# Optimization experiments

Measured on AMD Instinct MI355X. Metric: run time of the kernel, lower is better.

The kernel has to match this reference:

```python
import jax, jax.numpy as jnp
import numpy as np

BINS = 256
EPS = 1e-8


def _norm255(x):
    # (x - min) / (max - min) * 255, truncated to int (torch .int())
    mx = jnp.max(x, axis=(2, 3), keepdims=True)
    mn = jnp.min(x, axis=(2, 3), keepdims=True)
    return ((x - mn) / (mx - mn) * 255.0).astype(jnp.int32)


def _hist256(x):
    # x int32 [B,C,H,W] -> per-(b,c) 256-bin histogram [B,C,256] float32
    B, C = x.shape[0], x.shape[1]
    flat = x.reshape(B * C, -1)
    rows = jnp.arange(B * C)[:, None]
    h = jnp.zeros((B * C, BINS), jnp.float32).at[rows, flat].add(1.0)
    return h.reshape(B, C, BINS)


def _entropy(x):
    # faithful to Entropy(): p = hist / (H*W); h = -sum p*log(p+1e-8)
    B, C, H, W = x.shape
    p = _hist256(x) / (H * W)
    h = -jnp.sum(p * jnp.log(p + EPS), axis=2)
    return h[:, :, None, None]  # [B,C,1,1]


def _joint_entropy(x_p, x_ms):
    # Faithful to Joint_entropy's quirky count: for each (i,j) it counts pixels
    # where (x_ms==i AND x_p==j) OR (x_ms!=i AND x_p!=j).
    # count[i,j] = 2*J[i,j] + npix - hist_ms[i] - hist_p[j], J = joint histogram.
    B, C, H, W = x_ms.shape
    npix = H * W
    bins = jnp.arange(BINS)
    M = (x_ms.reshape(B, C, npix)[..., None] == bins).astype(jnp.float32)  # [B,C,P,256]
    P = (x_p.reshape(B, npix)[..., None] == bins).astype(jnp.float32)      # [B,P,256]
    J = jnp.einsum('bcpi,bpj->bcij', M, P)                                  # [B,C,256,256]
    hist_ms = jnp.sum(M, axis=2)  # [B,C,256]
    hist_p = jnp.sum(P, axis=1)   # [B,256]
    count = 2.0 * J + npix - hist_ms[:, :, :, None] - hist_p[:, None, None, :]
    p = count / float(BINS * BINS)  # original divides by 256*256, not npix
    h = -jnp.sum(p * jnp.log(p + EPS), axis=(2, 3))
    return h[:, :, None, None]  # [B,C,1,1]


def _channel(f_p, f_ms):
    B, C, H, W = f_p.shape
    f_p_m = jnp.mean(f_p, axis=1, keepdims=True)  # [B,1,H,W]
    # AdaptiveAvgPool2d((16,16)) with H,W divisible by 16 == block mean
    pooled = f_p.reshape(B, C, 16, H // 16, 16, W // 16).mean(axis=(3, 5))
    f_p_a = jnp.mean(pooled, axis=1, keepdims=True)  # [B,1,16,16]
    f_ms_n = _norm255(f_ms)
    f_p_m_n = _norm255(f_p_m)
    f_p_a_n = _norm255(f_p_a)
    h_ms = _entropy(f_ms_n)                 # [B,C,1,1]
    h_p = _entropy(f_p_m_n)                 # [B,1,1,1]
    h_ms_p = _joint_entropy(f_p_a_n, f_ms_n)  # [B,C,1,1]
    mi = h_p + h_ms - h_ms_p
    mi = jax.nn.softmax(mi, axis=1)  # nn.Softmax() on 4D -> dim=1
    return f_ms + f_ms * mi


def _similarity(f_p, f_ms):
    B, C, H, W = f_p.shape
    f_ms_u = jax.image.resize(f_ms, (B, C, H, W), method='bilinear')
    a = f_ms_u.reshape(B, C, -1)
    b = f_p.reshape(B, C, -1)
    a = a - jnp.mean(a, axis=2, keepdims=True)
    b = b - jnp.mean(b, axis=2, keepdims=True)
    na = jnp.sqrt(jnp.sum(a * a, axis=2))  # [B,C] (ms norms)
    nb = jnp.sqrt(jnp.sum(b * b, axis=2))  # [B,C] (p norms)
    s = jnp.einsum('bcp,bdp->bcd', a, b)   # [B,C,C]
    return s / ((na * nb) / 100.0)[:, :, None]


def _spatial(f_p, f_ms):
    B, C, H, W = f_p.shape
    s_m = _similarity(f_p, f_ms)
    mx = jnp.max(s_m, axis=2)        # [B,C]
    idx = jnp.argmax(s_m, axis=2)    # [B,C] best f_p channel per ms channel
    scores = jax.nn.softmax(mx, axis=1)
    brow = jnp.arange(B)[:, None]
    # group score: sum of softmax scores of ms-channels that picked value v
    g = jnp.zeros((B, C), scores.dtype).at[brow, idx].add(scores)
    cnt = jnp.zeros((B, C), jnp.int32).at[brow, idx].add(1)
    k = jnp.min(jnp.sum(cnt > 0, axis=1))  # min #unique over batch
    min_k = (k + 1) // 2                   # ceil(min_k / 2)
    order = jnp.argsort(-g, axis=1)        # descending group score; absent groups (0) sort last
    sorted_scores = jnp.take_along_axis(g, order, axis=1)  # [B,C]
    pos_mask = jnp.arange(C) < min_k       # keep top min_k positions
    z = jnp.where(pos_mask[None, :], sorted_scores, -jnp.inf)
    w = jax.nn.softmax(z, axis=1)          # softmax over selected scores, 0 elsewhere
    gathered = jnp.take_along_axis(f_p, order[:, :, None, None], axis=1)  # [B,C,H,W]
    mask = jnp.sum(w[:, :, None, None] * jax.nn.sigmoid(gathered), axis=1, keepdims=True)
    return f_p + f_p * mask


def setup_inputs() -> dict:
    key = jax.random.key(0)
    k1, k2 = jax.random.split(key)
    f_p = jax.random.normal(k1, (8, 64, 256, 256), dtype=jnp.float32)
    f_ms = jax.random.normal(k2, (8, 64, 16, 16), dtype=jnp.float32)
    return {"f_p": f_p, "f_ms": f_ms}


def reference(f_p, f_ms):
    rel_ms = _channel(f_p, f_ms)
    rel_p = _spatial(f_p, f_ms)
    return (rel_p, rel_ms)
```

## Files before the change

### kernel.cpp

```cpp
#include <hip/hip_runtime.h>

#define BB 8
#define CC 64
#define HP 256
#define WP 256
#define PP 65536
#define QQ 256

__device__ __forceinline__ unsigned encF(float f) {
    unsigned u = __float_as_uint(f);
    return (u & 0x80000000u) ? ~u : (u | 0x80000000u);
}
__device__ __forceinline__ float decF(unsigned u) {
    unsigned b = (u & 0x80000000u) ? (u ^ 0x80000000u) : ~u;
    return __uint_as_float(b);
}

__device__ __forceinline__ double blockSumD(double v, double* red4) {
    int t = threadIdx.x;
    for (int d = 32; d; d >>= 1) v += __shfl_down(v, d, 64);
    __syncthreads();
    if ((t & 63) == 0) red4[t >> 6] = v;
    __syncthreads();
    double r = red4[0] + red4[1] + red4[2] + red4[3];
    __syncthreads();
    return r;
}

__global__ void k0_init(unsigned* minmax, int* histpm) {
    int t = threadIdx.x + blockIdx.x * blockDim.x;
    if (t < BB) { minmax[2 * t] = 0xFFFFFFFFu; minmax[2 * t + 1] = 0u; }
    if (t < BB * 256) histpm[t] = 0;
}

__global__ __launch_bounds__(256) void k1_fpm(const float* __restrict__ fp,
                                              float* __restrict__ fpm,
                                              unsigned* __restrict__ minmax) {
    int b = blockIdx.y;
    int i4 = blockIdx.x * 256 + threadIdx.x;
    const float4* src = (const float4*)(fp + (size_t)b * CC * PP);
    float sx = 0.f, sy = 0.f, sz = 0.f, sw = 0.f;
#pragma unroll 8
    for (int c = 0; c < CC; ++c) {
        float4 v = src[(size_t)c * (PP / 4) + i4];
        sx += v.x; sy += v.y; sz += v.z; sw += v.w;
    }
    const float inv = 1.0f / 64.0f;
    float4 m; m.x = sx * inv; m.y = sy * inv; m.z = sz * inv; m.w = sw * inv;
    ((float4*)(fpm + (size_t)b * PP))[i4] = m;
    float mn = fminf(fminf(m.x, m.y), fminf(m.z, m.w));
    float mx = fmaxf(fmaxf(m.x, m.y), fmaxf(m.z, m.w));
    for (int d = 32; d; d >>= 1) {
        mn = fminf(mn, __shfl_down(mn, d, 64));
        mx = fmaxf(mx, __shfl_down(mx, d, 64));
    }
    __shared__ unsigned smn, smx;
    if (threadIdx.x == 0) { smn = 0xFFFFFFFFu; smx = 0u; }
    __syncthreads();
    if ((threadIdx.x & 63) == 0) { atomicMin(&smn, encF(mn)); atomicMax(&smx, encF(mx)); }
    __syncthreads();
    if (threadIdx.x == 0) { atomicMin(&minmax[2 * b], smn); atomicMax(&minmax[2 * b + 1], smx); }
}

__global__ __launch_bounds__(256) void k2a_hist(const float* __restrict__ fpm,
                                                const unsigned* __restrict__ minmax,
                                                int* __restrict__ histpm) {
    int b = blockIdx.y;
    __shared__ int h[256];
    h[threadIdx.x] = 0;
    __syncthreads();
    float mn = decF(minmax[2 * b]);
    float mx = decF(minmax[2 * b + 1]);
    float dd = mx - mn;
    int i4 = blockIdx.x * 256 + threadIdx.x;
    float4 v = ((const float4*)(fpm + (size_t)b * PP))[i4];
    int b0 = (int)((v.x - mn) / dd * 255.0f);
    int b1 = (int)((v.y - mn) / dd * 255.0f);
    int b2 = (int)((v.z - mn) / dd * 255.0f);
    int b3 = (int)((v.w - mn) / dd * 255.0f);
    b0 = min(max(b0, 0), 255); b1 = min(max(b1, 0), 255);
    b2 = min(max(b2, 0), 255); b3 = min(max(b3, 0), 255);
    atomicAdd(&h[b0], 1); atomicAdd(&h[b1], 1);
    atomicAdd(&h[b2], 1); atomicAdd(&h[b3], 1);
    __syncthreads();
    atomicAdd(&histpm[b * 256 + threadIdx.x], h[threadIdx.x]);
}

__global__ __launch_bounds__(256) void k2b_entropy(const int* __restrict__ histpm,
                                                   float* __restrict__ hpE) {
    __shared__ double red4[4];
    int b = blockIdx.x;
    int n = histpm[b * 256 + threadIdx.x];
    float p = (float)n * (1.0f / 65536.0f);
    double term = -(double)(p * __logf(p + 1e-8f));
    double h = blockSumD(term, red4);
    if (threadIdx.x == 0) hpE[b] = (float)h;
}

__global__ __launch_bounds__(256) void k3_chan(const float* __restrict__ fp,
                                               float* __restrict__ cellsum,
                                               float* __restrict__ gtent,
                                               float* __restrict__ chsum,
                                               float* __restrict__ chsumsq) {
    int blk = blockIdx.x, b = blk >> 6, c = blk & 63;
    int x = threadIdx.x, s = x >> 4, r = x & 15;
    const float* src = fp + (size_t)(b * CC + c) * PP;
    __shared__ float tentL[256];
    __shared__ double red4[4];
    tentL[x] = 0.0f;
    __syncthreads();
    float wm, w0, wp;
    if (x <= 7)        { wm = 0.f; w0 = 1.f; wp = 0.f; }
    else if (x >= 248) { wm = 0.f; w0 = 1.f; wp = 0.f; }
    else if (r < 8)    { float fx = ((float)r + 8.5f) * 0.0625f; wm = 1.f - fx; w0 = fx;       wp = 0.f; }
    else               { float fx = ((float)r - 7.5f) * 0.0625f; wm = 0.f;      w0 = 1.f - fx; wp = fx;  }
    double sum = 0.0, ssq = 0.0;
    for (int q = 0; q < 16; ++q) {
        float am = 0.f, a0 = 0.f, ap = 0.f, cs = 0.f;
#pragma unroll
        for (int ry = 0; ry < 16; ++ry) {
            float v = src[(q * 16 + ry) * 256 + x];
            sum += (double)v;
            ssq += (double)v * (double)v;
            cs  += v;
            if ((q == 0 && ry < 8) || (q == 15 && ry >= 8)) {
                a0 += v;
            } else if (ry < 8) {
                float fy = ((float)ry + 8.5f) * 0.0625f;
                am += (1.f - fy) * v; a0 += fy * v;
            } else {
                float fy = ((float)ry - 7.5f) * 0.0625f;
                a0 += (1.f - fy) * v; ap += fy * v;
            }
        }
        float vals[10];
        vals[0] = am * wm; vals[1] = am * w0; vals[2] = am * wp;
        vals[3] = a0 * wm; vals[4] = a0 * w0; vals[5] = a0 * wp;
        vals[6] = ap * wm; vals[7] = ap * w0; vals[8] = ap * wp;
        vals[9] = cs;
#pragma unroll
        for (int d = 8; d; d >>= 1) {
#pragma unroll
            for (int k2 = 0; k2 < 10; ++k2) vals[k2] += __shfl_down(vals[k2], d, 16);
        }
        if (r == 0) {
            if (q > 0) {
                if (s > 0)  atomicAdd(&tentL[(q - 1) * 16 + (s - 1)], vals[0]);
                atomicAdd(&tentL[(q - 1) * 16 + s], vals[1]);
                if (s < 15) atomicAdd(&tentL[(q - 1) * 16 + (s + 1)], vals[2]);
            }
            if (s > 0)  atomicAdd(&tentL[q * 16 + (s - 1)], vals[3]);
            atomicAdd(&tentL[q * 16 + s], vals[4]);
            if (s < 15) atomicAdd(&tentL[q * 16 + (s + 1)], vals[5]);
            if (q < 15) {
                if (s > 0)  atomicAdd(&tentL[(q + 1) * 16 + (s - 1)], vals[6]);
                atomicAdd(&tentL[(q + 1) * 16 + s], vals[7]);
                if (s < 15) atomicAdd(&tentL[(q + 1) * 16 + (s + 1)], vals[8]);
            }
            cellsum[(size_t)(b * CC + c) * QQ + q * 16 + s] = vals[9];
        }
    }
    __syncthreads();
    gtent[(size_t)(b * CC + c) * QQ + x] = tentL[x];
    double st = blockSumD(sum, red4);
    double sq = blockSumD(ssq, red4);
    if (x == 0) { chsum[b * CC + c] = (float)st; chsumsq[b * CC + c] = (float)sq; }
}

__global__ __launch_bounds__(256) void k4_ms(const float* __restrict__ fms,
                                             int* __restrict__ msn,
                                             int* __restrict__ histms,
                                             float* __restrict__ hmsE,
                                             float* __restrict__ naArr,
                                             float* __restrict__ mssum) {
    int blk = blockIdx.x, b = blk >> 6, c = blk & 63, t = threadIdx.x;
    __shared__ float m[256];
    __shared__ int hist[256];
    __shared__ double red4[4];
    __shared__ double U[256];
    __shared__ unsigned umn, umx;
    float v = fms[(size_t)(b * CC + c) * QQ + t];
    m[t] = v;
    hist[t] = 0;
    if (t == 0) { umn = 0xFFFFFFFFu; umx = 0u; }
    float mn = v, mx = v;
    for (int d = 32; d; d >>= 1) {
        mn = fminf(mn, __shfl_down(mn, d, 64));
        mx = fmaxf(mx, __shfl_down(mx, d, 64));
    }
    __syncthreads();
    if ((t & 63) == 0) { atomicMin(&umn, encF(mn)); atomicMax(&umx, encF(mx)); }
    __syncthreads();
    mn = decF(umn); mx = decF(umx);
    int bin = (int)((v - mn) / (mx - mn) * 255.0f);
    bin = min(max(bin, 0), 255);
    msn[(size_t)(b * CC + c) * QQ + t] = bin;
    atomicAdd(&hist[bin], 1);
    __syncthreads();
    histms[(size_t)(b * CC + c) * QQ + t] = hist[t];
    float pf = (float)hist[t] * (1.0f / 256.0f);
    double term = -(double)(pf * __logf(pf + 1e-8f));
    double h = blockSumD(term, red4);
    if (t == 0) hmsE[b * CC + c] = (float)h;
    int i = t >> 4, j = t & 15;
    double kdj = (j == 0 || j == 15) ? 13.328125 : 10.65625;
    double mv = (double)m[t];
    double uu = kdj * mv + 2.671875 * ((j > 0 ? (double)m[t - 1] : 0.0) +
                                       (j < 15 ? (double)m[t + 1] : 0.0));
    U[t] = uu;
    __syncthreads();
    double kdi = (i == 0 || i == 15) ? 13.328125 : 10.65625;
    double vv = kdi * U[t] + 2.671875 * ((i > 0 ? U[t - 16] : 0.0) +
                                         (i < 15 ? U[t + 16] : 0.0));
    double sq = blockSumD(mv * vv, red4);
    double msm = blockSumD(mv, red4);
    if (t == 0) {
        mssum[b * CC + c] = (float)msm;
        double meanu = msm * (1.0 / 256.0);
        double na2 = sq - 65536.0 * meanu * meanu;
        naArr[b * CC + c] = (float)sqrt(na2 > 0.0 ? na2 : 0.0);
    }
}

__global__ __launch_bounds__(256) void k5_pa(const float* __restrict__ cellsum,
                                             int* __restrict__ pan,
                                             int* __restrict__ histp) {
    int b = blockIdx.x, t = threadIdx.x;
    __shared__ int hist[256];
    __shared__ unsigned umn, umx;
    hist[t] = 0;
    if (t == 0) { umn = 0xFFFFFFFFu; umx = 0u; }
    double acc = 0.0;
    for (int c = 0; c < CC; ++c) acc += (double)cellsum[(size_t)(b * CC + c) * QQ + t];
    float pa = (float)(acc * (1.0 / 256.0) * (1.0 / 64.0));
    float mn = pa, mx = pa;
    for (int d = 32; d; d >>= 1) {
        mn = fminf(mn, __shfl_down(mn, d, 64));
        mx = fmaxf(mx, __shfl_down(mx, d, 64));
    }
    __syncthreads();
    if ((t & 63) == 0) { atomicMin(&umn, encF(mn)); atomicMax(&umx, encF(mx)); }
    __syncthreads();
    mn = decF(umn); mx = decF(umx);
    int bin = (int)((pa - mn) / (mx - mn) * 255.0f);
    bin = min(max(bin, 0), 255);
    pan[b * QQ + t] = bin;
    atomicAdd(&hist[bin], 1);
    __syncthreads();
    histp[b * 256 + t] = hist[t];
}

__global__ __launch_bounds__(256) void k6_joint(const int* __restrict__ msn,
                                                const int* __restrict__ pan,
                                                const int* __restrict__ histms,
                                                const int* __restrict__ histp,
                                                float* __restrict__ hjoint) {
    int blk = blockIdx.x, b = blk >> 6, c = blk & 63, t = threadIdx.x;
    __shared__ int key[256], hms[256], hp[256];
    __shared__ double red4[4];
    int iv = msn[(size_t)(b * CC + c) * QQ + t];
    int jv = pan[b * QQ + t];
    key[t] = (iv << 8) | jv;
    hms[t] = histms[(size_t)(b * CC + c) * QQ + t];
    hp[t] = histp[b * 256 + t];
    __syncthreads();
    unsigned long long w0_ = 0, w1_ = 0, w2_ = 0, w3_ = 0;
    for (int p = 0; p < 256; ++p) {
        int k2 = key[p];
        if ((k2 >> 8) == t) {
            int j = k2 & 255;
            unsigned long long bit = 1ull << (j & 63);
            int w = j >> 6;
            if (w == 0) w0_ |= bit; else if (w == 1) w1_ |= bit;
            else if (w == 2) w2_ |= bit; else w3_ |= bit;
        }
    }
    double acc = 0.0;
    int basei = 256 - hms[t];
    unsigned long long words[4] = { w0_, w1_, w2_, w3_ };
#pragma unroll
    for (int w = 0; w < 4; ++w) {
        unsigned long long word = words[w];
        for (int jj = 0; jj < 64; ++jj) {
            if (!((word >> jj) & 1ull)) {
                int cnt = basei - hp[w * 64 + jj];
                float pf = (float)cnt * (1.0f / 65536.0f);
                acc -= (double)(pf * __logf(pf + 1e-8f));
            }
        }
    }
    int myk = key[t], n = 0; bool first = true;
    for (int p = 0; p < 256; ++p) {
        int k2 = key[p];
        if (k2 == myk) { n++; if (p < t) first = false; }
    }
    if (first) {
        int cnt = 2 * n + 256 - hms[myk >> 8] - hp[myk & 255];
        float pf = (float)cnt * (1.0f / 65536.0f);
        acc -= (double)(pf * __logf(pf + 1e-8f));
    }
    double h = blockSumD(acc, red4);
    if (t == 0) hjoint[b * CC + c] = (float)h;
}

__global__ __launch_bounds__(256) void k7_relms(const float* __restrict__ fms,
                                                const float* __restrict__ hmsE,
                                                const float* __restrict__ hpE,
                                                const float* __restrict__ hjoint,
                                                float* __restrict__ out2) {
    int b = blockIdx.x, t = threadIdx.x;
    __shared__ double mi[64];
    if (t < 64) mi[t] = (double)hpE[b] + (double)hmsE[b * CC + t] - (double)hjoint[b * CC + t];
    __syncthreads();
    if (t == 0) {
        double mxv = mi[0];
        for (int c2 = 1; c2 < 64; ++c2) if (mi[c2] > mxv) mxv = mi[c2];
        double s = 0.0;
        for (int c2 = 0; c2 < 64; ++c2) { mi[c2] = exp(mi[c2] - mxv); s += mi[c2]; }
        for (int c2 = 0; c2 < 64; ++c2) mi[c2] /= s;
    }
    __syncthreads();
    const float* src = fms + (size_t)b * CC * QQ;
    float* dst = out2 + (size_t)b * CC * QQ;
    for (int e = t; e < CC * QQ; e += 256) {
        float v = src[e];
        float miv = (float)mi[e >> 8];
        dst[e] = v + v * miv;
    }
}

__global__ __launch_bounds__(256) void k8_smax(const float* __restrict__ fms,
                                               const float* __restrict__ gtent,
                                               const float* __restrict__ mssum,
                                               const float* __restrict__ chsum,
                                               const float* __restrict__ chsumsq,
                                               const float* __restrict__ naArr,
                                               float* __restrict__ mxArr,
                                               int* __restrict__ idxArr) {
    int blk = blockIdx.x, b = blk >> 6, c = blk & 63, t = threadIdx.x;
    __shared__ float msrow[256];
    __shared__ double part[256];
    __shared__ double sval[64];
    msrow[t] = fms[(size_t)(b * CC + c) * QQ + t];
    __syncthreads();
    int d = t >> 2, pr = t & 3;
    const float* g = gtent + (size_t)(b * CC + d) * QQ + pr * 64;
    const float* mr = msrow + pr * 64;
    double acc = 0.0;
    for (int q2 = 0; q2 < 64; ++q2) acc += (double)mr[q2] * (double)g[q2];
    part[t] = acc;
    __syncthreads();
    if (t < 64) {
        double meanu = (double)mssum[b * CC + c] * (1.0 / 256.0);
        double meanp = (double)chsum[b * CC + t] * (1.0 / 65536.0);
        sval[t] = part[t * 4] + part[t * 4 + 1] + part[t * 4 + 2] + part[t * 4 + 3]
                  - 65536.0 * meanu * meanp;
    }
    __syncthreads();
    if (t == 0) {
        double best = sval[0]; int bi2 = 0;
        for (int dd = 1; dd < 64; ++dd) { if (sval[dd] > best) { best = sval[dd]; bi2 = dd; } }
        double nac = (double)naArr[b * CC + c];
        double sc_ = (double)chsum[b * CC + c];
        double sq_ = (double)chsumsq[b * CC + c];
        double nb2 = sq_ - sc_ * sc_ * (1.0 / 65536.0);
        double nbc = sqrt(nb2 > 0.0 ? nb2 : 0.0);
        mxArr[b * CC + c] = (float)(best * 100.0 / (nac * nbc));
        idxArr[b * CC + c] = bi2;
    }
}

__global__ __launch_bounds__(512) void k9_small(const float* __restrict__ mxArr,
                                                const int* __restrict__ idxArr,
                                                float* __restrict__ wsel,
                                                int* __restrict__ chanA,
                                                int* __restrict__ minkA) {
    __shared__ double sc[8][64];
    __shared__ double gs[8][64];
    __shared__ int idxS[8][64];
    __shared__ int ordv[8][64];
    __shared__ int uarr[8];
    __shared__ int mkS;
    int t = threadIdx.x;
    int b = t >> 6, c = t & 63;
    double v = (double)mxArr[b * 64 + c];
    double mx = v;
    for (int d = 32; d; d >>= 1) mx = fmax(mx, __shfl_down(mx, d, 64));
    mx = __shfl(mx, 0, 64);
    double e = exp(v - mx);
    double s = e;
    for (int d = 32; d; d >>= 1) s += __shfl_down(s, d, 64);
    s = __shfl(s, 0, 64);
    sc[b][c] = e / s;
    idxS[b][c] = idxArr[b * 64 + c];
    __syncthreads();
    double g = 0.0; int cnt = 0;
    for (int c2 = 0; c2 < 64; ++c2) {
        if (idxS[b][c2] == c) { g += sc[b][c2]; cnt++; }
    }
    gs[b][c] = g;
    unsigned long long ball = __ballot(cnt > 0);
    if (c == 0) uarr[b] = __popcll(ball);
    __syncthreads();
    if (t == 0) {
        int k = uarr[0];
        for (int b2 = 1; b2 < 8; ++b2) k = min(k, uarr[b2]);
        mkS = (k + 1) >> 1;
        minkA[0] = mkS;
    }
    __syncthreads();
    int rk = 0;
    double myg = gs[b][c];
    for (int c3 = 0; c3 < 64; ++c3) {
        double a = gs[b][c3];
        if (a > myg || (a == myg && c3 < c)) rk++;
    }
    ordv[b][rk] = c;
    __syncthreads();
    int mk = mkS;
    double z0 = gs[b][ordv[b][0]];
    double ee = (c < mk) ? exp(gs[b][ordv[b][c]] - z0) : 0.0;
    double se = ee;
    for (int d = 32; d; d >>= 1) se += __shfl_down(se, d, 64);
    se = __shfl(se, 0, 64);
    if (c < mk) {
        wsel[b * 64 + c] = (float)(ee / se);
        chanA[b * 64 + c] = ordv[b][c];
    }
}

__global__ __launch_bounds__(256) void k10_relp(const float* __restrict__ fp,
                                                const float* __restrict__ wsel,
                                                const int* __restrict__ chanA,
                                                const int* __restrict__ minkA,
                                                float* __restrict__ outp) {
    int b = blockIdx.y;
    int i4 = blockIdx.x * 256 + threadIdx.x;
    int mk = minkA[0];
    const float4* src = (const float4*)(fp + (size_t)b * CC * PP);
    float mx0 = 0.f, mx1 = 0.f, mx2 = 0.f, mx3 = 0.f;
    for (int i = 0; i < mk; ++i) {
        int ch = chanA[b * 64 + i];
        float wv = wsel[b * 64 + i];
        float4 v = src[(size_t)ch * (PP / 4) + i4];
        mx0 += wv * (1.0f / (1.0f + __expf(-v.x)));
        mx1 += wv * (1.0f / (1.0f + __expf(-v.y)));
        mx2 += wv * (1.0f / (1.0f + __expf(-v.z)));
        mx3 += wv * (1.0f / (1.0f + __expf(-v.w)));
    }
    float4* dst = (float4*)(outp + (size_t)b * CC * PP);
    for (int c2 = 0; c2 < CC; ++c2) {
        float4 v = src[(size_t)c2 * (PP / 4) + i4];
        float4 o;
        o.x = v.x + v.x * mx0;
        o.y = v.y + v.y * mx1;
        o.z = v.z + v.z * mx2;
        o.w = v.w + v.w * mx3;
        dst[(size_t)c2 * (PP / 4) + i4] = o;
    }
}

extern "C" void kernel_launch(void* const* d_in, const int* in_sizes, int n_in,
                              void* d_out, int out_size, void* d_ws, size_t ws_size,
                              hipStream_t stream) {
    const float* fp = (const float*)d_in[0];
    const float* fms = (const float*)d_in[1];
    float* out = (float*)d_out;

    char* p = (char*)d_ws;
    auto alloc = [&](size_t bytes) { void* r = (void*)p; p += (bytes + 255) & ~(size_t)255; return r; };

    float* fpm      = (float*)alloc((size_t)BB * PP * 4);
    float* cellsum  = (float*)alloc((size_t)BB * CC * QQ * 4);
    float* gtent    = (float*)alloc((size_t)BB * CC * QQ * 4);
    float* chsum    = (float*)alloc((size_t)BB * CC * 4);
    float* chsumsq  = (float*)alloc((size_t)BB * CC * 4);
    unsigned* minmax= (unsigned*)alloc((size_t)BB * 2 * 4);
    int* histpm     = (int*)alloc((size_t)BB * 256 * 4);
    int* msn        = (int*)alloc((size_t)BB * CC * QQ * 4);
    int* histms     = (int*)alloc((size_t)BB * CC * 256 * 4);
    int* histp      = (int*)alloc((size_t)BB * 256 * 4);
    int* pan        = (int*)alloc((size_t)BB * QQ * 4);
    float* hmsE     = (float*)alloc((size_t)BB * CC * 4);
    float* hpE      = (float*)alloc((size_t)BB * 4);
    float* hjoint   = (float*)alloc((size_t)BB * CC * 4);
    float* naArr    = (float*)alloc((size_t)BB * CC * 4);
    float* mssum    = (float*)alloc((size_t)BB * CC * 4);
    float* mxArr    = (float*)alloc((size_t)BB * CC * 4);
    int* idxArr     = (int*)alloc((size_t)BB * CC * 4);
    float* wsel     = (float*)alloc((size_t)BB * CC * 4);
    int* chanA      = (int*)alloc((size_t)BB * CC * 4);
    int* minkA      = (int*)alloc(256);

    float* out_relp  = out;
    float* out_relms = out + (size_t)BB * CC * PP;

    k0_init<<<8, 256, 0, stream>>>(minmax, histpm);
    k1_fpm<<<dim3(64, 8), 256, 0, stream>>>(fp, fpm, minmax);
    k2a_hist<<<dim3(64, 8), 256, 0, stream>>>(fpm, minmax, histpm);
    k2b_entropy<<<8, 256, 0, stream>>>(histpm, hpE);
    k3_chan<<<512, 256, 0, stream>>>(fp, cellsum, gtent, chsum, chsumsq);
    k4_ms<<<512, 256, 0, stream>>>(fms, msn, histms, hmsE, naArr, mssum);
    k5_pa<<<8, 256, 0, stream>>>(cellsum, pan, histp);
    k6_joint<<<512, 256, 0, stream>>>(msn, pan, histms, histp, hjoint);
    k7_relms<<<8, 256, 0, stream>>>(fms, hmsE, hpE, hjoint, out_relms);
    k8_smax<<<512, 256, 0, stream>>>(fms, gtent, mssum, chsum, chsumsq, naArr, mxArr, idxArr);
    k9_small<<<1, 512, 0, stream>>>(mxArr, idxArr, wsel, chanA, minkA);
    k10_relp<<<dim3(64, 8), 256, 0, stream>>>(fp, wsel, chanA, minkA, out_relp);
}
```

Baseline: 416.7 us.

## Fuse channel-mean pass into relp output kernel and merge small histogram kernels

```diff
diff --git a/kernel.cpp b/kernel.cpp
--- a/kernel.cpp
+++ b/kernel.cpp
@@ -27,74 +27,9 @@
     return r;
 }
 
-__global__ void k0_init(unsigned* minmax, int* histpm) {
-    int t = threadIdx.x + blockIdx.x * blockDim.x;
+__global__ __launch_bounds__(256) void k0_init(unsigned* __restrict__ minmax) {
+    int t = threadIdx.x;
     if (t < BB) { minmax[2 * t] = 0xFFFFFFFFu; minmax[2 * t + 1] = 0u; }
-    if (t < BB * 256) histpm[t] = 0;
-}
-
-__global__ __launch_bounds__(256) void k1_fpm(const float* __restrict__ fp,
-                                              float* __restrict__ fpm,
-                                              unsigned* __restrict__ minmax) {
-    int b = blockIdx.y;
-    int i4 = blockIdx.x * 256 + threadIdx.x;
-    const float4* src = (const float4*)(fp + (size_t)b * CC * PP);
-    float sx = 0.f, sy = 0.f, sz = 0.f, sw = 0.f;
-#pragma unroll 8
-    for (int c = 0; c < CC; ++c) {
-        float4 v = src[(size_t)c * (PP / 4) + i4];
-        sx += v.x; sy += v.y; sz += v.z; sw += v.w;
-    }
-    const float inv = 1.0f / 64.0f;
-    float4 m; m.x = sx * inv; m.y = sy * inv; m.z = sz * inv; m.w = sw * inv;
-    ((float4*)(fpm + (size_t)b * PP))[i4] = m;
-    float mn = fminf(fminf(m.x, m.y), fminf(m.z, m.w));
-    float mx = fmaxf(fmaxf(m.x, m.y), fmaxf(m.z, m.w));
-    for (int d = 32; d; d >>= 1) {
-        mn = fminf(mn, __shfl_down(mn, d, 64));
-        mx = fmaxf(mx, __shfl_down(mx, d, 64));
-    }
-    __shared__ unsigned smn, smx;
-    if (threadIdx.x == 0) { smn = 0xFFFFFFFFu; smx = 0u; }
-    __syncthreads();
-    if ((threadIdx.x & 63) == 0) { atomicMin(&smn, encF(mn)); atomicMax(&smx, encF(mx)); }
-    __syncthreads();
-    if (threadIdx.x == 0) { atomicMin(&minmax[2 * b], smn); atomicMax(&minmax[2 * b + 1], smx); }
-}
-
-__global__ __launch_bounds__(256) void k2a_hist(const float* __restrict__ fpm,
-                                                const unsigned* __restrict__ minmax,
-                                                int* __restrict__ histpm) {
-    int b = blockIdx.y;
-    __shared__ int h[256];
-    h[threadIdx.x] = 0;
-    __syncthreads();
-    float mn = decF(minmax[2 * b]);
-    float mx = decF(minmax[2 * b + 1]);
-    float dd = mx - mn;
-    int i4 = blockIdx.x * 256 + threadIdx.x;
-    float4 v = ((const float4*)(fpm + (size_t)b * PP))[i4];
-    int b0 = (int)((v.x - mn) / dd * 255.0f);
-    int b1 = (int)((v.y - mn) / dd * 255.0f);
-    int b2 = (int)((v.z - mn) / dd * 255.0f);
-    int b3 = (int)((v.w - mn) / dd * 255.0f);
-    b0 = min(max(b0, 0), 255); b1 = min(max(b1, 0), 255);
-    b2 = min(max(b2, 0), 255); b3 = min(max(b3, 0), 255);
-    atomicAdd(&h[b0], 1); atomicAdd(&h[b1], 1);
-    atomicAdd(&h[b2], 1); atomicAdd(&h[b3], 1);
-    __syncthreads();
-    atomicAdd(&histpm[b * 256 + threadIdx.x], h[threadIdx.x]);
-}
-
-__global__ __launch_bounds__(256) void k2b_entropy(const int* __restrict__ histpm,
-                                                   float* __restrict__ hpE) {
-    __shared__ double red4[4];
-    int b = blockIdx.x;
-    int n = histpm[b * 256 + threadIdx.x];
-    float p = (float)n * (1.0f / 65536.0f);
-    double term = -(double)(p * __logf(p + 1e-8f));
-    double h = blockSumD(term, red4);
-    if (threadIdx.x == 0) hpE[b] = (float)h;
 }
 
 __global__ __launch_bounds__(256) void k3_chan(const float* __restrict__ fp,
@@ -222,113 +157,6 @@
     }
 }
 
-__global__ __launch_bounds__(256) void k5_pa(const float* __restrict__ cellsum,
-                                             int* __restrict__ pan,
-                                             int* __restrict__ histp) {
-    int b = blockIdx.x, t = threadIdx.x;
-    __shared__ int hist[256];
-    __shared__ unsigned umn, umx;
-    hist[t] = 0;
-    if (t == 0) { umn = 0xFFFFFFFFu; umx = 0u; }
-    double acc = 0.0;
-    for (int c = 0; c < CC; ++c) acc += (double)cellsum[(size_t)(b * CC + c) * QQ + t];
-    float pa = (float)(acc * (1.0 / 256.0) * (1.0 / 64.0));
-    float mn = pa, mx = pa;
-    for (int d = 32; d; d >>= 1) {
-        mn = fminf(mn, __shfl_down(mn, d, 64));
-        mx = fmaxf(mx, __shfl_down(mx, d, 64));
-    }
-    __syncthreads();
-    if ((t & 63) == 0) { atomicMin(&umn, encF(mn)); atomicMax(&umx, encF(mx)); }
-    __syncthreads();
-    mn = decF(umn); mx = decF(umx);
-    int bin = (int)((pa - mn) / (mx - mn) * 255.0f);
-    bin = min(max(bin, 0), 255);
-    pan[b * QQ + t] = bin;
-    atomicAdd(&hist[bin], 1);
-    __syncthreads();
-    histp[b * 256 + t] = hist[t];
-}
-
-__global__ __launch_bounds__(256) void k6_joint(const int* __restrict__ msn,
-                                                const int* __restrict__ pan,
-                                                const int* __restrict__ histms,
-                                                const int* __restrict__ histp,
-                                                float* __restrict__ hjoint) {
-    int blk = blockIdx.x, b = blk >> 6, c = blk & 63, t = threadIdx.x;
-    __shared__ int key[256], hms[256], hp[256];
-    __shared__ double red4[4];
-    int iv = msn[(size_t)(b * CC + c) * QQ + t];
-    int jv = pan[b * QQ + t];
-    key[t] = (iv << 8) | jv;
-    hms[t] = histms[(size_t)(b * CC + c) * QQ + t];
-    hp[t] = histp[b * 256 + t];
-    __syncthreads();
-    unsigned long long w0_ = 0, w1_ = 0, w2_ = 0, w3_ = 0;
-    for (int p = 0; p < 256; ++p) {
-        int k2 = key[p];
-        if ((k2 >> 8) == t) {
-            int j = k2 & 255;
-            unsigned long long bit = 1ull << (j & 63);
-            int w = j >> 6;
-            if (w == 0) w0_ |= bit; else if (w == 1) w1_ |= bit;
-            else if (w == 2) w2_ |= bit; else w3_ |= bit;
-        }
-    }
-    double acc = 0.0;
-    int basei = 256 - hms[t];
-    unsigned long long words[4] = { w0_, w1_, w2_, w3_ };
-#pragma unroll
-    for (int w = 0; w < 4; ++w) {
-        unsigned long long word = words[w];
-        for (int jj = 0; jj < 64; ++jj) {
-            if (!((word >> jj) & 1ull)) {
-                int cnt = basei - hp[w * 64 + jj];
-                float pf = (float)cnt * (1.0f / 65536.0f);
-                acc -= (double)(pf * __logf(pf + 1e-8f));
-            }
-        }
-    }
-    int myk = key[t], n = 0; bool first = true;
-    for (int p = 0; p < 256; ++p) {
-        int k2 = key[p];
-        if (k2 == myk) { n++; if (p < t) first = false; }
-    }
-    if (first) {
-        int cnt = 2 * n + 256 - hms[myk >> 8] - hp[myk & 255];
-        float pf = (float)cnt * (1.0f / 65536.0f);
-        acc -= (double)(pf * __logf(pf + 1e-8f));
-    }
-    double h = blockSumD(acc, red4);
-    if (t == 0) hjoint[b * CC + c] = (float)h;
-}
-
-__global__ __launch_bounds__(256) void k7_relms(const float* __restrict__ fms,
-                                                const float* __restrict__ hmsE,
-                                                const float* __restrict__ hpE,
-                                                const float* __restrict__ hjoint,
-                                                float* __restrict__ out2) {
-    int b = blockIdx.x, t = threadIdx.x;
-    __shared__ double mi[64];
-    if (t < 64) mi[t] = (double)hpE[b] + (double)hmsE[b * CC + t] - (double)hjoint[b * CC + t];
-    __syncthreads();
-    if (t == 0) {
-        double mxv = mi[0];
-        for (int c2 = 1; c2 < 64; ++c2) if (mi[c2] > mxv) mxv = mi[c2];
-        double s = 0.0;
-        for (int c2 = 0; c2 < 64; ++c2) { mi[c2] = exp(mi[c2] - mxv); s += mi[c2]; }
-        for (int c2 = 0; c2 < 64; ++c2) mi[c2] /= s;
-    }
-    __syncthreads();
-    const float* src = fms + (size_t)b * CC * QQ;
-    float* dst = out2 + (size_t)b * CC * QQ;
-    for (int e = t; e < CC * QQ; e += 256) {
-        float v = src[e];
-        float miv = (float)mi[e >> 8];
-        dst[e] = v + v * miv;
-    }
-}
-
 __global__ __launch_bounds__(256) void k8_smax(const float* __restrict__ fms,
                                                const float* __restrict__ gtent,
                                                const float* __restrict__ mssum,
@@ -433,7 +261,9 @@
                                                 const float* __restrict__ wsel,
                                                 const int* __restrict__ chanA,
                                                 const int* __restrict__ minkA,
-                                                float* __restrict__ outp) {
+                                                float* __restrict__ outp,
+                                                float* __restrict__ fpm,
+                                                unsigned* __restrict__ minmax) {
     int b = blockIdx.y;
     int i4 = blockIdx.x * 256 + threadIdx.x;
     int mk = minkA[0];
@@ -448,9 +278,11 @@
         mx2 += wv * (1.0f / (1.0f + __expf(-v.z)));
         mx3 += wv * (1.0f / (1.0f + __expf(-v.w)));
     }
+    float sx = 0.f, sy = 0.f, sz = 0.f, sw = 0.f;
     float4* dst = (float4*)(outp + (size_t)b * CC * PP);
     for (int c2 = 0; c2 < CC; ++c2) {
         float4 v = src[(size_t)c2 * (PP / 4) + i4];
+        sx += v.x; sy += v.y; sz += v.z; sw += v.w;
         float4 o;
         o.x = v.x + v.x * mx0;
         o.y = v.y + v.y * mx1;
@@ -458,6 +290,157 @@
         o.w = v.w + v.w * mx3;
         dst[(size_t)c2 * (PP / 4) + i4] = o;
     }
+    const float inv = 1.0f / 64.0f;
+    float4 m; m.x = sx * inv; m.y = sy * inv; m.z = sz * inv; m.w = sw * inv;
+    ((float4*)(fpm + (size_t)b * PP))[i4] = m;
+    float mn = fminf(fminf(m.x, m.y), fminf(m.z, m.w));
+    float mxv = fmaxf(fmaxf(m.x, m.y), fmaxf(m.z, m.w));
+    for (int d = 32; d; d >>= 1) {
+        mn = fminf(mn, __shfl_down(mn, d, 64));
+        mxv = fmaxf(mxv, __shfl_down(mxv, d, 64));
+    }
+    __shared__ unsigned smn, smx;
+    if (threadIdx.x == 0) { smn = 0xFFFFFFFFu; smx = 0u; }
+    __syncthreads();
+    if ((threadIdx.x & 63) == 0) { atomicMin(&smn, encF(mn)); atomicMax(&smx, encF(mxv)); }
+    __syncthreads();
+    if (threadIdx.x == 0) { atomicMin(&minmax[2 * b], smn); atomicMax(&minmax[2 * b + 1], smx); }
+}
+
+__global__ __launch_bounds__(256) void kC_small(const float* __restrict__ fpm,
+                                                const unsigned* __restrict__ minmax,
+                                                const float* __restrict__ cellsum,
+                                                float* __restrict__ hpE,
+                                                int* __restrict__ pan,
+                                                int* __restrict__ histp) {
+    int b = blockIdx.x, t = threadIdx.x;
+    __shared__ int hist[256];
+    __shared__ double red4[4];
+    __shared__ unsigned umn, umx;
+    hist[t] = 0;
+    if (t == 0) { umn = 0xFFFFFFFFu; umx = 0u; }
+    __syncthreads();
+    float mn = decF(minmax[2 * b]);
+    float mx = decF(minmax[2 * b + 1]);
+    float dd = mx - mn;
+    const float4* src = (const float4*)(fpm + (size_t)b * PP);
+    for (int i4 = t; i4 < PP / 4; i4 += 256) {
+        float4 v = src[i4];
+        int b0 = (int)((v.x - mn) / dd * 255.0f);
+        int b1 = (int)((v.y - mn) / dd * 255.0f);
+        int b2 = (int)((v.z - mn) / dd * 255.0f);
+        int b3 = (int)((v.w - mn) / dd * 255.0f);
+        b0 = min(max(b0, 0), 255); b1 = min(max(b1, 0), 255);
+        b2 = min(max(b2, 0), 255); b3 = min(max(b3, 0), 255);
+        atomicAdd(&hist[b0], 1); atomicAdd(&hist[b1], 1);
+        atomicAdd(&hist[b2], 1); atomicAdd(&hist[b3], 1);
+    }
+    __syncthreads();
+    int n = hist[t];
+    float p = (float)n * (1.0f / 65536.0f);
+    double term = -(double)(p * __logf(p + 1e-8f));
+    double h = blockSumD(term, red4);
+    if (t == 0) hpE[b] = (float)h;
+    __syncthreads();
+    hist[t] = 0;
+    __syncthreads();
+    double acc = 0.0;
+    for (int c = 0; c < CC; ++c) acc += (double)cellsum[(size_t)(b * CC + c) * QQ + t];
+    float pa = (float)(acc * (1.0 / 256.0) * (1.0 / 64.0));
+    float mn2 = pa, mx2 = pa;
+    for (int d = 32; d; d >>= 1) {
+        mn2 = fminf(mn2, __shfl_down(mn2, d, 64));
+        mx2 = fmaxf(mx2, __shfl_down(mx2, d, 64));
+    }
+    __syncthreads();
+    if ((t & 63) == 0) { atomicMin(&umn, encF(mn2)); atomicMax(&umx, encF(mx2)); }
+    __syncthreads();
+    mn2 = decF(umn); mx2 = decF(umx);
+    int bin = (int)((pa - mn2) / (mx2 - mn2) * 255.0f);
+    bin = min(max(bin, 0), 255);
+    pan[b * QQ + t] = bin;
+    atomicAdd(&hist[bin], 1);
+    __syncthreads();
+    histp[b * 256 + t] = hist[t];
+}
+
+__global__ __launch_bounds__(256) void k6_joint(const int* __restrict__ msn,
+                                                const int* __restrict__ pan,
+                                                const int* __restrict__ histms,
+                                                const int* __restrict__ histp,
+                                                float* __restrict__ hjoint) {
+    int blk = blockIdx.x, b = blk >> 6, c = blk & 63, t = threadIdx.x;
+    __shared__ int key[256], hms[256], hp[256];
+    __shared__ double red4[4];
+    int iv = msn[(size_t)(b * CC + c) * QQ + t];
+    int jv = pan[b * QQ + t];
+    key[t] = (iv << 8) | jv;
+    hms[t] = histms[(size_t)(b * CC + c) * QQ + t];
+    hp[t] = histp[b * 256 + t];
+    __syncthreads();
+    unsigned long long w0_ = 0, w1_ = 0, w2_ = 0, w3_ = 0;
+    for (int p = 0; p < 256; ++p) {
+        int k2 = key[p];
+        if ((k2 >> 8) == t) {
+            int j = k2 & 255;
+            unsigned long long bit = 1ull << (j & 63);
+            int w = j >> 6;
+            if (w == 0) w0_ |= bit; else if (w == 1) w1_ |= bit;
+            else if (w == 2) w2_ |= bit; else w3_ |= bit;
+        }
+    }
+    double acc = 0.0;
+    int basei = 256 - hms[t];
+    unsigned long long words[4] = { w0_, w1_, w2_, w3_ };
+#pragma unroll
+    for (int w = 0; w < 4; ++w) {
+        unsigned long long word = words[w];
+        for (int jj = 0; jj < 64; ++jj) {
+            if (!((word >> jj) & 1ull)) {
+                int cnt = basei - hp[w * 64 + jj];
+                float pf = (float)cnt * (1.0f / 65536.0f);
+                acc -= (double)(pf * __logf(pf + 1e-8f));
+            }
+        }
+    }
+    int myk = key[t], n = 0; bool first = true;
+    for (int p = 0; p < 256; ++p) {
+        int k2 = key[p];
+        if (k2 == myk) { n++; if (p < t) first = false; }
+    }
+    if (first) {
+        int cnt = 2 * n + 256 - hms[myk >> 8] - hp[myk & 255];
+        float pf = (float)cnt * (1.0f / 65536.0f);
+        acc -= (double)(pf * __logf(pf + 1e-8f));
+    }
+    double h = blockSumD(acc, red4);
+    if (t == 0) hjoint[b * CC + c] = (float)h;
+}
+
+__global__ __launch_bounds__(256) void k7_relms(const float* __restrict__ fms,
+                                                const float* __restrict__ hmsE,
+                                                const float* __restrict__ hpE,
+                                                const float* __restrict__ hjoint,
+                                                float* __restrict__ out2) {
+    int b = blockIdx.x, t = threadIdx.x;
+    __shared__ double mi[64];
+    if (t < 64) mi[t] = (double)hpE[b] + (double)hmsE[b * CC + t] - (double)hjoint[b * CC + t];
+    __syncthreads();
+    if (t == 0) {
+        double mxv = mi[0];
+        for (int c2 = 1; c2 < 64; ++c2) if (mi[c2] > mxv) mxv = mi[c2];
+        double s = 0.0;
+        for (int c2 = 0; c2 < 64; ++c2) { mi[c2] = exp(mi[c2] - mxv); s += mi[c2]; }
+        for (int c2 = 0; c2 < 64; ++c2) mi[c2] /= s;
+    }
+    __syncthreads();
+    const float* src = fms + (size_t)b * CC * QQ;
+    float* dst = out2 + (size_t)b * CC * QQ;
+    for (int e = t; e < CC * QQ; e += 256) {
+        float v = src[e];
+        float miv = (float)mi[e >> 8];
+        dst[e] = v + v * miv;
+    }
 }
 
 extern "C" void kernel_launch(void* const* d_in, const int* in_sizes, int n_in,
@@ -476,7 +459,6 @@
     float* chsum    = (float*)alloc((size_t)BB * CC * 4);
     float* chsumsq  = (float*)alloc((size_t)BB * CC * 4);
     unsigned* minmax= (unsigned*)alloc((size_t)BB * 2 * 4);
-    int* histpm     = (int*)alloc((size_t)BB * 256 * 4);
     int* msn        = (int*)alloc((size_t)BB * CC * QQ * 4);
     int* histms     = (int*)alloc((size_t)BB * CC * 256 * 4);
     int* histp      = (int*)alloc((size_t)BB * 256 * 4);
@@ -495,16 +477,13 @@
     float* out_relp  = out;
     float* out_relms = out + (size_t)BB * CC * PP;
 
-    k0_init<<<8, 256, 0, stream>>>(minmax, histpm);
-    k1_fpm<<<dim3(64, 8), 256, 0, stream>>>(fp, fpm, minmax);
-    k2a_hist<<<dim3(64, 8), 256, 0, stream>>>(fpm, minmax, histpm);
-    k2b_entropy<<<8, 256, 0, stream>>>(histpm, hpE);
+    k0_init<<<1, 256, 0, stream>>>(minmax);
     k3_chan<<<512, 256, 0, stream>>>(fp, cellsum, gtent, chsum, chsumsq);
     k4_ms<<<512, 256, 0, stream>>>(fms, msn, histms, hmsE, naArr, mssum);
-    k5_pa<<<8, 256, 0, stream>>>(cellsum, pan, histp);
+    k8_smax<<<512, 256, 0, stream>>>(fms, gtent, mssum, chsum, chsumsq, naArr, mxArr, idxArr);
+    k9_small<<<1, 512, 0, stream>>>(mxArr, idxArr, wsel, chanA, minkA);
+    k10_relp<<<dim3(64, 8), 256, 0, stream>>>(fp, wsel, chanA, minkA, out_relp, fpm, minmax);
+    kC_small<<<8, 256, 0, stream>>>(fpm, minmax, cellsum, hpE, pan, histp);
     k6_joint<<<512, 256, 0, stream>>>(msn, pan, histms, histp, hjoint);
     k7_relms<<<8, 256, 0, stream>>>(fms, hmsE, hpE, hjoint, out_relms);
-    k8_smax<<<512, 256, 0, stream>>>(fms, gtent, mssum, chsum, chsumsq, naArr, mxArr, idxArr);
-    k9_small<<<1, 512, 0, stream>>>(mxArr, idxArr, wsel, chanA, minkA);
-    k10_relp<<<dim3(64, 8), 256, 0, stream>>>(fp, wsel, chanA, minkA, out_relp);
-}
+}
```

New measurement: 420.9 us. No clear change (+1.0%).
